# Kernel tuning notes

Measured on AMD Instinct MI355X. Metric: run time of the kernel, lower is better.

The kernel has to match this reference:

```python
import jax, jax.numpy as jnp
import numpy as np

N_ASSETS = 512
WINDOW = 256
BATCH = 32
THRESHOLDS = (0.3, 0.5, 0.7)
N_SQUARINGS = 9  # ceil(log2(N_ASSETS)); reachability converges after log2(n) squarings


def setup_inputs() -> dict:
    key = jax.random.key(0)
    returns = jax.random.normal(key, (BATCH, WINDOW, N_ASSETS), dtype=jnp.float32)
    return {"returns": returns}


def _betti_features(corr):
    """corr: (B, N, N). Returns (B, 2*len(THRESHOLDS)) Betti features."""
    B, N, _ = corr.shape
    eye = jnp.eye(N, dtype=jnp.float32)
    idx = jnp.arange(N)
    feats = []
    for t in THRESHOLDS:
        # adjacency with zeroed diagonal (matches np.fill_diagonal(adj, 0))
        adj = (jnp.abs(corr) > t).astype(jnp.float32) * (1.0 - eye)
        # transitive closure via repeated boolean squaring of (A | I)
        R = jnp.minimum(adj + eye, 1.0)
        for _ in range(N_SQUARINGS):
            R = (jnp.einsum('bij,bjk->bik', R, R) > 0).astype(jnp.float32)
        # component representative of node i = smallest reachable index;
        # number of components = count of self-representatives
        comp_rep = jnp.argmax(R, axis=-1)              # first 1 along row = min index
        components = jnp.sum(comp_rep == idx[None, :], axis=-1).astype(jnp.float32)
        edges = jnp.sum(adj, axis=(-1, -2)) / 2.0
        betti0 = components
        betti1 = jnp.maximum(0.0, edges - N + components)
        feats.append(betti0 / N)
        feats.append(betti1 / N)
    return jnp.stack(feats, axis=-1)  # (B, 2*n_thresholds), order [t0_b0, t0_b1, t1_b0, ...]


def reference(returns) -> jnp.ndarray:
    B, W, N = returns.shape
    ret_centered = returns - returns.mean(axis=1, keepdims=True)
    # torch .std() is unbiased (ddof=1)
    std = jnp.std(ret_centered, axis=1, keepdims=True, ddof=1) + 1e-8
    ret_normalized = ret_centered / std
    corr = jnp.einsum('bwi,bwj->bij', ret_normalized, ret_normalized) / W
    return _betti_features(corr)
```

## Files before the change

kernel.cpp:

```cpp
#include <hip/hip_runtime.h>
#include <hip/hip_bf16.h>
#include <stdint.h>

#define NASSETS 512
#define WINDOW  256
#define NBATCH  32
#define NWORDS  16
#define BM 128
#define BN 128
#define BK 64

typedef __attribute__((ext_vector_type(4))) float floatx4;
typedef __attribute__((ext_vector_type(8))) short shortx8;

__device__ __forceinline__ unsigned short f2bf(float f) {
    union { float f; unsigned int u; } c; c.f = f;
    unsigned int u = c.u;
    unsigned int r = (u + 0x7FFFu + ((u >> 16) & 1u)) >> 16;
    return (unsigned short)r;
}

__device__ __forceinline__ void gload16(const void* gp, void* lp) {
    __builtin_amdgcn_global_load_lds(
        (const __attribute__((address_space(1))) void*)(uintptr_t)gp,
        (__attribute__((address_space(3))) void*)(unsigned int)(uintptr_t)lp,
        16, 0, 0);
}

__global__ __launch_bounds__(512)
void normalize_kernel(const float* __restrict__ ret, short* __restrict__ Xt) {
    __shared__ float sred[512];
    __shared__ float ssred[512];
    __shared__ float smean[64];
    __shared__ float sinv[64];
    __shared__ __align__(16) short tile[64 * 256];

    const int t  = threadIdx.x;
    const int a  = t & 63;
    const int wc = t >> 6;
    const int g  = blockIdx.x;
    const int b  = blockIdx.y;
    const int n0 = g * 64;

    const float* base = ret + (size_t)b * WINDOW * NASSETS + n0 + a;

    float x[32];
    float s1 = 0.f, s2 = 0.f;
#pragma unroll
    for (int k = 0; k < 32; ++k) {
        x[k] = base[(size_t)(wc * 32 + k) * NASSETS];
        s1 += x[k];
        s2 += x[k] * x[k];
    }
    sred[wc * 64 + a]  = s1;
    ssred[wc * 64 + a] = s2;
    __syncthreads();

    if (t < 64) {
        float S = 0.f, S2 = 0.f;
#pragma unroll
        for (int c = 0; c < 8; ++c) { S += sred[c * 64 + t]; S2 += ssred[c * 64 + t]; }
        float mean = S / (float)WINDOW;
        float var  = (S2 - (float)WINDOW * mean * mean) / (float)(WINDOW - 1);
        if (var < 0.f) var = 0.f;
        float stdv = sqrtf(var) + 1e-8f;
        smean[t] = mean;
        sinv[t]  = 1.0f / stdv;
    }
    __syncthreads();

    const float m  = smean[a];
    const float iv = sinv[a];

#pragma unroll
    for (int kslot = 0; kslot < 4; ++kslot) {
        shortx8 pk;
#pragma unroll
        for (int j = 0; j < 8; ++j)
            pk[j] = (short)f2bf((x[kslot * 8 + j] - m) * iv);
        int s = wc * 4 + kslot;
        int sp = s ^ (a & 7);
        *(shortx8*)(tile + a * 256 + sp * 8) = pk;
    }
    __syncthreads();

    short* orow = Xt + ((size_t)b * NASSETS + n0) * WINDOW;
#pragma unroll
    for (int it = 0; it < 4; ++it) {
        int seg = it * 512 + t;
        int r = seg >> 5;
        int s = seg & 31;
        shortx8 v = *(const shortx8*)(tile + r * 256 + (s ^ (r & 7)) * 8);
        *(shortx8*)(orow + r * WINDOW + s * 8) = v;
    }
}

__global__ __launch_bounds__(256)
void corr_adj_kernel(const short* __restrict__ Xt, unsigned int* __restrict__ adj) {
    __shared__ __align__(16) short lsA[BM * BK];
    __shared__ __align__(16) short lsB[BN * BK];

    const int t    = threadIdx.x;
    const int lane = t & 63;
    const int wave = t >> 6;
    const int wi   = wave >> 1, wj = wave & 1;
    const int b  = blockIdx.z;
    const int i0 = blockIdx.y * BM;
    const int j0 = blockIdx.x * BN;

    const short* base = Xt + (size_t)b * NASSETS * WINDOW;

    const int m = lane & 15;
    const int q = lane >> 4;

    const int srowAdd  = lane >> 3;
    const int gsegOffS = ((lane & 7) ^ (lane >> 3)) * 8;

    floatx4 acc[4][4] = {};

    for (int k0 = 0; k0 < WINDOW; k0 += BK) {
        __syncthreads();
#pragma unroll
        for (int tt = 0; tt < 4; ++tt) {
            int ro = wave * 32 + tt * 8 + srowAdd;
            const short* gA = base + (size_t)(i0 + ro) * WINDOW + k0 + gsegOffS;
            const short* gB = base + (size_t)(j0 + ro) * WINDOW + k0 + gsegOffS;
            char* dA = (char*)lsA + (wave * 32 + tt * 8) * (BK * 2);
            char* dB = (char*)lsB + (wave * 32 + tt * 8) * (BK * 2);
            gload16(gA, dA);
            gload16(gB, dB);
        }
        __syncthreads();

#pragma unroll
        for (int kk = 0; kk < 2; ++kk) {
            const int slot = ((kk * 4 + q) ^ (lane & 7)) * 16;
            shortx8 af[4], bf[4];
#pragma unroll
            for (int mi = 0; mi < 4; ++mi)
                af[mi] = *(const shortx8*)((char*)lsA + (wi * 64 + mi * 16 + m) * (BK * 2) + slot);
#pragma unroll
            for (int nj = 0; nj < 4; ++nj)
                bf[nj] = *(const shortx8*)((char*)lsB + (wj * 64 + nj * 16 + m) * (BK * 2) + slot);
#pragma unroll
            for (int mi = 0; mi < 4; ++mi)
#pragma unroll
                for (int nj = 0; nj < 4; ++nj)
                    acc[mi][nj] = __builtin_amdgcn_mfma_f32_16x16x32_bf16(
                        af[mi], bf[nj], acc[mi][nj], 0, 0, 0);
        }
    }

    const float T[3] = {0.3f * (float)WINDOW, 0.5f * (float)WINDOW, 0.7f * (float)WINDOW};
    unsigned int wout[3][2] = {{0u,0u},{0u,0u},{0u,0u}};
    const int qp = (lane >> 2) & 3;
#pragma unroll
    for (int mi = 0; mi < 4; ++mi) {
#pragma unroll
        for (int r = 0; r < 4; ++r) {
            bool act = ((lane >> 4) == mi) && ((lane & 3) == r);
#pragma unroll
            for (int th = 0; th < 3; ++th) {
                unsigned long long b0 = __ballot(fabsf(acc[mi][0][r]) > T[th]);
                unsigned long long b1 = __ballot(fabsf(acc[mi][1][r]) > T[th]);
                unsigned long long b2 = __ballot(fabsf(acc[mi][2][r]) > T[th]);
                unsigned long long b3 = __ballot(fabsf(acc[mi][3][r]) > T[th]);
                if (act) {
                    wout[th][0] = ((unsigned int)(b0 >> (qp * 16)) & 0xFFFFu)
                                | (((unsigned int)(b1 >> (qp * 16)) & 0xFFFFu) << 16);
                    wout[th][1] = ((unsigned int)(b2 >> (qp * 16)) & 0xFFFFu)
                                | (((unsigned int)(b3 >> (qp * 16)) & 0xFFFFu) << 16);
                }
            }
        }
    }

    const int grow    = i0 + wi * 64 + lane;
    const int colbase = j0 + wj * 64;
    unsigned int dd = (unsigned int)(grow - colbase);
    if (dd < 64u) {
        unsigned int m0 = (dd < 32u) ? ~(1u << dd) : 0xFFFFFFFFu;
        unsigned int m1 = (dd >= 32u) ? ~(1u << (dd - 32u)) : 0xFFFFFFFFu;
#pragma unroll
        for (int th = 0; th < 3; ++th) { wout[th][0] &= m0; wout[th][1] &= m1; }
    }
    const int wb = colbase >> 5;
    const size_t stride_t = (size_t)NBATCH * NASSETS * NWORDS;
    size_t rb = ((size_t)b * NASSETS + grow) * NWORDS + wb;
#pragma unroll
    for (int th = 0; th < 3; ++th) {
        adj[rb + th * stride_t]     = wout[th][0];
        adj[rb + th * stride_t + 1] = wout[th][1];
    }
}

__global__ __launch_bounds__(512)
void betti_kernel(const unsigned int* __restrict__ adj, float* __restrict__ out) {
    __shared__ int lab[NASSETS];
    __shared__ int changed;
    __shared__ int red[8];

    int th = blockIdx.x;
    int b  = blockIdx.y;
    int i  = threadIdx.x;
    int lane = i & 63, wv = i >> 6;

    const unsigned int* rowp =
        adj + (((size_t)th * NBATCH + b) * NASSETS + i) * NWORDS;
    unsigned int row[NWORDS];
    int deg = 0;
#pragma unroll
    for (int w = 0; w < NWORDS; ++w) {
        row[w] = rowp[w];
        deg += __popc(row[w]);
    }

    int v = deg;
#pragma unroll
    for (int off = 32; off > 0; off >>= 1) v += __shfl_down(v, off);
    if (lane == 0) red[wv] = v;
    lab[i] = i;
    __syncthreads();
    int total_deg = 0;
    if (i == 0)
        for (int k = 0; k < 8; ++k) total_deg += red[k];

    for (;;) {
        __syncthreads();
        if (i == 0) changed = 0;
        __syncthreads();
        int mlab = lab[i];
#pragma unroll
        for (int w = 0; w < NWORDS; ++w) {
            unsigned int bits = row[w];
            int basej = w * 32;
            while (bits) {
                int j = basej + __builtin_ctz(bits);
                bits &= bits - 1;
                int lj = lab[j];
                if (lj < mlab) mlab = lj;
            }
        }
        int lm = lab[mlab];
        if (lm < mlab) mlab = lm;
        __syncthreads();
        if (mlab < lab[i]) { lab[i] = mlab; changed = 1; }
        __syncthreads();
        if (!changed) break;
    }

    int isrep = (lab[i] == i) ? 1 : 0;
#pragma unroll
    for (int off = 32; off > 0; off >>= 1) isrep += __shfl_down(isrep, off);
    if (lane == 0) red[wv] = isrep;
    __syncthreads();
    if (i == 0) {
        int comps = 0;
        for (int k = 0; k < 8; ++k) comps += red[k];
        float compf = (float)comps;
        float edges = (float)total_deg * 0.5f;
        float b0 = compf / (float)NASSETS;
        float b1 = fmaxf(0.0f, edges - (float)NASSETS + compf) / (float)NASSETS;
        out[b * 6 + th * 2 + 0] = b0;
        out[b * 6 + th * 2 + 1] = b1;
    }
}

extern "C" void kernel_launch(void* const* d_in, const int* in_sizes, int n_in,
                              void* d_out, int out_size, void* d_ws, size_t ws_size,
                              hipStream_t stream) {
    const float* ret = (const float*)d_in[0];
    float* out = (float*)d_out;
    char* ws = (char*)d_ws;

    short* Xt = (short*)ws;
    unsigned int* adj =
        (unsigned int*)(ws + (size_t)NBATCH * NASSETS * WINDOW * sizeof(short));

    dim3 g1(NASSETS / 64, NBATCH);
    normalize_kernel<<<g1, 512, 0, stream>>>(ret, Xt);

    dim3 g2(NASSETS / BN, NASSETS / BM, NBATCH);
    corr_adj_kernel<<<g2, 256, 0, stream>>>(Xt, adj);

    dim3 g3(3, NBATCH);
    betti_kernel<<<g3, 512, 0, stream>>>(adj, out);
}
```

Baseline: 80.20 us.

## Fuse correlation and component counting per batch with FP8 MFMA

Normalized returns are now quantized to FP8 E4M3 instead of bf16, and the correlation GEMM uses fp8 MFMA instructions. The correlation/adjacency kernel and the Betti connected-components kernel are merged into one kernel with one block per batch. This removes a launch and halves input bytes. The cost is only 32 blocks of parallelism for the GEMM on a large GPU, plus lower precision that could flip edges near the thresholds.

```diff
diff --git a/kernel.cpp b/kernel.cpp
--- a/kernel.cpp
+++ b/kernel.cpp
@@ -6,34 +6,51 @@
 #define WINDOW  256
 #define NBATCH  32
 #define NWORDS  16
-#define BM 128
-#define BN 128
-#define BK 64
+#define XSTRIDE 80
 
 typedef __attribute__((ext_vector_type(4))) float floatx4;
-typedef __attribute__((ext_vector_type(8))) short shortx8;
-
-__device__ __forceinline__ unsigned short f2bf(float f) {
-    union { float f; unsigned int u; } c; c.f = f;
-    unsigned int u = c.u;
-    unsigned int r = (u + 0x7FFFu + ((u >> 16) & 1u)) >> 16;
-    return (unsigned short)r;
-}
-
-__device__ __forceinline__ void gload16(const void* gp, void* lp) {
-    __builtin_amdgcn_global_load_lds(
-        (const __attribute__((address_space(1))) void*)(uintptr_t)gp,
-        (__attribute__((address_space(3))) void*)(unsigned int)(uintptr_t)lp,
-        16, 0, 0);
+typedef __attribute__((ext_vector_type(4))) int   intx4;
+typedef __attribute__((ext_vector_type(2))) long  longx2;
+
+__device__ __forceinline__ unsigned int f2e4m3_manual(float x) {
+    union { float f; unsigned u; } c; c.f = x;
+    unsigned s = (c.u >> 24) & 0x80u;
+    unsigned a = c.u & 0x7FFFFFFFu;
+    float af = fabsf(x);
+    unsigned code;
+    if (af >= 448.f) code = 0x7Eu;
+    else if (af < 0.015625f) {
+        code = (unsigned)(int)rintf(af * 512.f);
+    } else {
+        unsigned E = a >> 23;
+        unsigned base = ((E - 120u) << 3) | ((a >> 20) & 7u);
+        unsigned rem = a & 0xFFFFFu;
+        if (rem > 0x80000u || (rem == 0x80000u && (base & 1u))) base++;
+        if (base > 0x7Eu) base = 0x7Eu;
+        code = base;
+    }
+    return s | code;
+}
+
+__device__ __forceinline__ int pack4fp8(float f0, float f1, float f2, float f3) {
+#if defined(__has_builtin) && __has_builtin(__builtin_amdgcn_cvt_pk_fp8_f32)
+    int v = 0;
+    v = __builtin_amdgcn_cvt_pk_fp8_f32(f0, f1, v, false);
+    v = __builtin_amdgcn_cvt_pk_fp8_f32(f2, f3, v, true);
+    return v;
+#else
+    return (int)(f2e4m3_manual(f0) | (f2e4m3_manual(f1) << 8) |
+                 (f2e4m3_manual(f2) << 16) | (f2e4m3_manual(f3) << 24));
+#endif
 }
 
 __global__ __launch_bounds__(512)
-void normalize_kernel(const float* __restrict__ ret, short* __restrict__ Xt) {
+void normalize_kernel(const float* __restrict__ ret, char* __restrict__ Xt) {
     __shared__ float sred[512];
     __shared__ float ssred[512];
     __shared__ float smean[64];
     __shared__ float sinv[64];
-    __shared__ __align__(16) short tile[64 * 256];
+    __shared__ __align__(16) char tile[64 * 256];
 
     const int t  = threadIdx.x;
     const int a  = t & 63;
@@ -69,200 +86,187 @@
     }
     __syncthreads();
 
-    const float m  = smean[a];
+    const float mn = smean[a];
     const float iv = sinv[a];
 
-#pragma unroll
-    for (int kslot = 0; kslot < 4; ++kslot) {
-        shortx8 pk;
-#pragma unroll
-        for (int j = 0; j < 8; ++j)
-            pk[j] = (short)f2bf((x[kslot * 8 + j] - m) * iv);
-        int s = wc * 4 + kslot;
-        int sp = s ^ (a & 7);
-        *(shortx8*)(tile + a * 256 + sp * 8) = pk;
-    }
+    int pk[8];
+#pragma unroll
+    for (int j = 0; j < 8; ++j)
+        pk[j] = pack4fp8((x[4*j+0] - mn) * iv, (x[4*j+1] - mn) * iv,
+                         (x[4*j+2] - mn) * iv, (x[4*j+3] - mn) * iv);
+    char* rowp = tile + a * 256;
+    intx4 lo = {pk[0], pk[1], pk[2], pk[3]};
+    intx4 hi = {pk[4], pk[5], pk[6], pk[7]};
+    *(intx4*)(rowp + ((wc * 2 + 0) ^ (a & 15)) * 16) = lo;
+    *(intx4*)(rowp + ((wc * 2 + 1) ^ (a & 15)) * 16) = hi;
     __syncthreads();
 
-    short* orow = Xt + ((size_t)b * NASSETS + n0) * WINDOW;
-#pragma unroll
-    for (int it = 0; it < 4; ++it) {
-        int seg = it * 512 + t;
-        int r = seg >> 5;
-        int s = seg & 31;
-        shortx8 v = *(const shortx8*)(tile + r * 256 + (s ^ (r & 7)) * 8);
-        *(shortx8*)(orow + r * WINDOW + s * 8) = v;
-    }
-}
-
-__global__ __launch_bounds__(256)
-void corr_adj_kernel(const short* __restrict__ Xt, unsigned int* __restrict__ adj) {
-    __shared__ __align__(16) short lsA[BM * BK];
-    __shared__ __align__(16) short lsB[BN * BK];
+    char* orow = Xt + ((size_t)b * NASSETS + n0) * WINDOW;
+#pragma unroll
+    for (int it = 0; it < 2; ++it) {
+        int idx = it * 512 + t;
+        int r = idx >> 4;
+        int s = idx & 15;
+        intx4 v = *(const intx4*)(tile + r * 256 + (s ^ (r & 15)) * 16);
+        *(intx4*)(orow + r * WINDOW + s * 16) = v;
+    }
+}
+
+__global__ __launch_bounds__(512)
+void fused_corr_cc_kernel(const char* __restrict__ Xt, unsigned int* __restrict__ adjG,
+                          float* __restrict__ out) {
+    __shared__ __align__(16) char Xs[NASSETS * XSTRIDE];
+    __shared__ int lab[NASSETS];
+    __shared__ int red[8];
+    __shared__ int changed;
 
     const int t    = threadIdx.x;
     const int lane = t & 63;
     const int wave = t >> 6;
-    const int wi   = wave >> 1, wj = wave & 1;
-    const int b  = blockIdx.z;
-    const int i0 = blockIdx.y * BM;
-    const int j0 = blockIdx.x * BN;
-
-    const short* base = Xt + (size_t)b * NASSETS * WINDOW;
-
-    const int m = lane & 15;
-    const int q = lane >> 4;
-
-    const int srowAdd  = lane >> 3;
-    const int gsegOffS = ((lane & 7) ^ (lane >> 3)) * 8;
-
-    floatx4 acc[4][4] = {};
-
-    for (int k0 = 0; k0 < WINDOW; k0 += BK) {
-        __syncthreads();
-#pragma unroll
-        for (int tt = 0; tt < 4; ++tt) {
-            int ro = wave * 32 + tt * 8 + srowAdd;
-            const short* gA = base + (size_t)(i0 + ro) * WINDOW + k0 + gsegOffS;
-            const short* gB = base + (size_t)(j0 + ro) * WINDOW + k0 + gsegOffS;
-            char* dA = (char*)lsA + (wave * 32 + tt * 8) * (BK * 2);
-            char* dB = (char*)lsB + (wave * 32 + tt * 8) * (BK * 2);
-            gload16(gA, dA);
-            gload16(gB, dB);
-        }
-        __syncthreads();
-
-#pragma unroll
-        for (int kk = 0; kk < 2; ++kk) {
-            const int slot = ((kk * 4 + q) ^ (lane & 7)) * 16;
-            shortx8 af[4], bf[4];
+    const int b    = blockIdx.x;
+    const int R0   = wave * 64;
+
+    const int m  = lane & 15;
+    const int kq = lane >> 4;
+
+    const float T[3] = {0.3f * (float)WINDOW, 0.5f * (float)WINDOW, 0.7f * (float)WINDOW};
+    const char* xbase = Xt + ((size_t)b * NASSETS) * WINDOW;
+
+    for (int j0 = 0; j0 < NASSETS; j0 += 128) {
+        floatx4 acc[4][8] = {};
+
+        for (int k0 = 0; k0 < WINDOW; k0 += 64) {
+            __syncthreads();
+#pragma unroll
+            for (int it = 0; it < 4; ++it) {
+                int idx = it * 512 + t;
+                int n   = idx >> 2;
+                int c   = idx & 3;
+                longx2 v = *(const longx2*)(xbase + (size_t)n * WINDOW + k0 + c * 16);
+                int q0 = (2 * c) & 3, q1 = (2 * c + 1) & 3;
+                int h  = (c >> 1) & 1;
+                char* rp = Xs + n * XSTRIDE;
+                *(long*)(rp + ((q0 ^ (n & 3)) * 16) + h * 8) = v.x;
+                *(long*)(rp + ((q1 ^ (n & 3)) * 16) + h * 8) = v.y;
+            }
+            __syncthreads();
+
+            longx2 af[4], bf[8];
+#pragma unroll
+            for (int mi = 0; mi < 4; ++mi) {
+                int n = R0 + mi * 16 + m;
+                af[mi] = *(const longx2*)(Xs + n * XSTRIDE + ((kq ^ (n & 3)) * 16));
+            }
+#pragma unroll
+            for (int nj = 0; nj < 8; ++nj) {
+                int n = j0 + nj * 16 + m;
+                bf[nj] = *(const longx2*)(Xs + n * XSTRIDE + ((kq ^ (n & 3)) * 16));
+            }
 #pragma unroll
             for (int mi = 0; mi < 4; ++mi)
-                af[mi] = *(const shortx8*)((char*)lsA + (wi * 64 + mi * 16 + m) * (BK * 2) + slot);
-#pragma unroll
-            for (int nj = 0; nj < 4; ++nj)
-                bf[nj] = *(const shortx8*)((char*)lsB + (wj * 64 + nj * 16 + m) * (BK * 2) + slot);
-#pragma unroll
-            for (int mi = 0; mi < 4; ++mi)
-#pragma unroll
-                for (int nj = 0; nj < 4; ++nj)
-                    acc[mi][nj] = __builtin_amdgcn_mfma_f32_16x16x32_bf16(
-                        af[mi], bf[nj], acc[mi][nj], 0, 0, 0);
-        }
-    }
-
-    const float T[3] = {0.3f * (float)WINDOW, 0.5f * (float)WINDOW, 0.7f * (float)WINDOW};
-    unsigned int wout[3][2] = {{0u,0u},{0u,0u},{0u,0u}};
-    const int qp = (lane >> 2) & 3;
-#pragma unroll
-    for (int mi = 0; mi < 4; ++mi) {
-#pragma unroll
-        for (int r = 0; r < 4; ++r) {
-            bool act = ((lane >> 4) == mi) && ((lane & 3) == r);
-#pragma unroll
-            for (int th = 0; th < 3; ++th) {
-                unsigned long long b0 = __ballot(fabsf(acc[mi][0][r]) > T[th]);
-                unsigned long long b1 = __ballot(fabsf(acc[mi][1][r]) > T[th]);
-                unsigned long long b2 = __ballot(fabsf(acc[mi][2][r]) > T[th]);
-                unsigned long long b3 = __ballot(fabsf(acc[mi][3][r]) > T[th]);
-                if (act) {
-                    wout[th][0] = ((unsigned int)(b0 >> (qp * 16)) & 0xFFFFu)
-                                | (((unsigned int)(b1 >> (qp * 16)) & 0xFFFFu) << 16);
-                    wout[th][1] = ((unsigned int)(b2 >> (qp * 16)) & 0xFFFFu)
-                                | (((unsigned int)(b3 >> (qp * 16)) & 0xFFFFu) << 16);
+#pragma unroll
+                for (int nj = 0; nj < 8; ++nj) {
+                    acc[mi][nj] = __builtin_amdgcn_mfma_f32_16x16x32_fp8_fp8(
+                        af[mi].x, bf[nj].x, acc[mi][nj], 0, 0, 0);
+                    acc[mi][nj] = __builtin_amdgcn_mfma_f32_16x16x32_fp8_fp8(
+                        af[mi].y, bf[nj].y, acc[mi][nj], 0, 0, 0);
                 }
-            }
-        }
-    }
-
-    const int grow    = i0 + wi * 64 + lane;
-    const int colbase = j0 + wj * 64;
-    unsigned int dd = (unsigned int)(grow - colbase);
-    if (dd < 64u) {
-        unsigned int m0 = (dd < 32u) ? ~(1u << dd) : 0xFFFFFFFFu;
-        unsigned int m1 = (dd >= 32u) ? ~(1u << (dd - 32u)) : 0xFFFFFFFFu;
-#pragma unroll
-        for (int th = 0; th < 3; ++th) { wout[th][0] &= m0; wout[th][1] &= m1; }
-    }
-    const int wb = colbase >> 5;
-    const size_t stride_t = (size_t)NBATCH * NASSETS * NWORDS;
-    size_t rb = ((size_t)b * NASSETS + grow) * NWORDS + wb;
-#pragma unroll
+        }
+
+        unsigned int wrd[3][4];
+        const int myMi = lane >> 4, myQp = (lane >> 2) & 3, myR = lane & 3;
+#pragma unroll
+        for (int mi = 0; mi < 4; ++mi)
+#pragma unroll
+            for (int r = 0; r < 4; ++r) {
+                bool act = (myMi == mi) && (myR == r);
+#pragma unroll
+                for (int th = 0; th < 3; ++th)
+#pragma unroll
+                    for (int jw = 0; jw < 4; ++jw) {
+                        unsigned long long blo = __ballot(fabsf(acc[mi][2*jw][r])   > T[th]);
+                        unsigned long long bhi = __ballot(fabsf(acc[mi][2*jw+1][r]) > T[th]);
+                        if (act)
+                            wrd[th][jw] = ((unsigned)(blo >> (myQp * 16)) & 0xFFFFu)
+                                        | (((unsigned)(bhi >> (myQp * 16)) & 0xFFFFu) << 16);
+                    }
+            }
+
+        const int grow = R0 + lane;
+        int dd = grow - j0;
+        if (dd >= 0 && dd < 128) {
+            unsigned mask = ~(1u << (dd & 31));
+            int w = dd >> 5;
+#pragma unroll
+            for (int th = 0; th < 3; ++th) wrd[th][w] &= mask;
+        }
+#pragma unroll
+        for (int th = 0; th < 3; ++th) {
+            size_t rbase = ((size_t)(th * NBATCH + b) * NASSETS + grow) * NWORDS + (j0 >> 5);
+#pragma unroll
+            for (int jw = 0; jw < 4; ++jw) adjG[rbase + jw] = wrd[th][jw];
+        }
+    }
+
+    const int lane6 = t & 63, wv = t >> 6;
     for (int th = 0; th < 3; ++th) {
-        adj[rb + th * stride_t]     = wout[th][0];
-        adj[rb + th * stride_t + 1] = wout[th][1];
-    }
-}
-
-__global__ __launch_bounds__(512)
-void betti_kernel(const unsigned int* __restrict__ adj, float* __restrict__ out) {
-    __shared__ int lab[NASSETS];
-    __shared__ int changed;
-    __shared__ int red[8];
-
-    int th = blockIdx.x;
-    int b  = blockIdx.y;
-    int i  = threadIdx.x;
-    int lane = i & 63, wv = i >> 6;
-
-    const unsigned int* rowp =
-        adj + (((size_t)th * NBATCH + b) * NASSETS + i) * NWORDS;
-    unsigned int row[NWORDS];
-    int deg = 0;
-#pragma unroll
-    for (int w = 0; w < NWORDS; ++w) {
-        row[w] = rowp[w];
-        deg += __popc(row[w]);
-    }
-
-    int v = deg;
-#pragma unroll
-    for (int off = 32; off > 0; off >>= 1) v += __shfl_down(v, off);
-    if (lane == 0) red[wv] = v;
-    lab[i] = i;
-    __syncthreads();
-    int total_deg = 0;
-    if (i == 0)
-        for (int k = 0; k < 8; ++k) total_deg += red[k];
-
-    for (;;) {
-        __syncthreads();
-        if (i == 0) changed = 0;
-        __syncthreads();
-        int mlab = lab[i];
+        __syncthreads();
+        const unsigned int* rowp = adjG + ((size_t)(th * NBATCH + b) * NASSETS + t) * NWORDS;
+        unsigned int row[NWORDS];
+        int deg = 0;
 #pragma unroll
         for (int w = 0; w < NWORDS; ++w) {
-            unsigned int bits = row[w];
-            int basej = w * 32;
-            while (bits) {
-                int j = basej + __builtin_ctz(bits);
-                bits &= bits - 1;
-                int lj = lab[j];
-                if (lj < mlab) mlab = lj;
-            }
-        }
-        int lm = lab[mlab];
-        if (lm < mlab) mlab = lm;
-        __syncthreads();
-        if (mlab < lab[i]) { lab[i] = mlab; changed = 1; }
-        __syncthreads();
-        if (!changed) break;
-    }
-
-    int isrep = (lab[i] == i) ? 1 : 0;
-#pragma unroll
-    for (int off = 32; off > 0; off >>= 1) isrep += __shfl_down(isrep, off);
-    if (lane == 0) red[wv] = isrep;
-    __syncthreads();
-    if (i == 0) {
-        int comps = 0;
-        for (int k = 0; k < 8; ++k) comps += red[k];
-        float compf = (float)comps;
-        float edges = (float)total_deg * 0.5f;
-        float b0 = compf / (float)NASSETS;
-        float b1 = fmaxf(0.0f, edges - (float)NASSETS + compf) / (float)NASSETS;
-        out[b * 6 + th * 2 + 0] = b0;
-        out[b * 6 + th * 2 + 1] = b1;
+            row[w] = rowp[w];
+            deg += __popc(row[w]);
+        }
+        int v = deg;
+#pragma unroll
+        for (int off = 32; off > 0; off >>= 1) v += __shfl_down(v, off);
+        if (lane6 == 0) red[wv] = v;
+        lab[t] = t;
+        __syncthreads();
+        int total_deg = 0;
+        if (t == 0)
+            for (int k = 0; k < 8; ++k) total_deg += red[k];
+
+        for (;;) {
+            __syncthreads();
+            if (t == 0) changed = 0;
+            __syncthreads();
+            int mlab = lab[t];
+#pragma unroll
+            for (int w = 0; w < NWORDS; ++w) {
+                unsigned int bits = row[w];
+                int basej = w * 32;
+                while (bits) {
+                    int j = basej + __builtin_ctz(bits);
+                    bits &= bits - 1;
+                    int lj = lab[j];
+                    if (lj < mlab) mlab = lj;
+                }
+            }
+            int lm = lab[mlab];
+            if (lm < mlab) mlab = lm;
+            __syncthreads();
+            if (mlab < lab[t]) { lab[t] = mlab; changed = 1; }
+            __syncthreads();
+            if (!changed) break;
+        }
+
+        int isrep = (lab[t] == t) ? 1 : 0;
+#pragma unroll
+        for (int off = 32; off > 0; off >>= 1) isrep += __shfl_down(isrep, off);
+        __syncthreads();
+        if (lane6 == 0) red[wv] = isrep;
+        __syncthreads();
+        if (t == 0) {
+            int comps = 0;
+            for (int k = 0; k < 8; ++k) comps += red[k];
+            float compf = (float)comps;
+            float edges = (float)total_deg * 0.5f;
+            out[b * 6 + th * 2 + 0] = compf / (float)NASSETS;
+            out[b * 6 + th * 2 + 1] = fmaxf(0.0f, edges - (float)NASSETS + compf) / (float)NASSETS;
+        }
     }
 }
 
@@ -273,16 +277,12 @@
     float* out = (float*)d_out;
     char* ws = (char*)d_ws;
 
-    short* Xt = (short*)ws;
-    unsigned int* adj =
-        (unsigned int*)(ws + (size_t)NBATCH * NASSETS * WINDOW * sizeof(short));
+    char* Xt = ws;
+    unsigned int* adjG =
+        (unsigned int*)(ws + (size_t)NBATCH * NASSETS * WINDOW);
 
     dim3 g1(NASSETS / 64, NBATCH);
     normalize_kernel<<<g1, 512, 0, stream>>>(ret, Xt);
 
-    dim3 g2(NASSETS / BN, NASSETS / BM, NBATCH);
-    corr_adj_kernel<<<g2, 256, 0, stream>>>(Xt, adj);
-
-    dim3 g3(3, NBATCH);
-    betti_kernel<<<g3, 512, 0, stream>>>(adj, out);
-}
+    fused_corr_cc_kernel<<<NBATCH, 512, 0, stream>>>(Xt, adjG, out);
+}
```

Result: slower. 130.3 us (+62.5%).
